# Kernel optimization log

Measured on AMD Instinct MI355X. Metric: run time of the kernel, lower is better.

Reference implementation:

```python
import jax, jax.numpy as jnp
import numpy as np

N_CLUSTERS = 64
N_GHOST = 2
EPS = 1e-12  # F.normalize eps


def setup_inputs() -> dict:
    key = jax.random.key(0)
    k1, k2, k3, k4 = jax.random.split(key, 4)
    n_utts, feat_dim, duration = 16, 256, 1500
    x = jax.random.normal(k1, (n_utts, feat_dim, duration), dtype=jnp.float32)
    centroids = jax.random.uniform(k2, (N_CLUSTERS, feat_dim), dtype=jnp.float32)
    # NetVLAD init ties linear.weight = 2*alpha*centroids(+ghosts); here independent params suffice for a math baseline
    lin_w = jax.random.normal(k3, (N_CLUSTERS + N_GHOST, feat_dim), dtype=jnp.float32)
    lin_b = jax.random.normal(k4, (N_CLUSTERS + N_GHOST,), dtype=jnp.float32)
    return {"x": x, "centroids": centroids, "lin_w": lin_w, "lin_b": lin_b}


def reference(x, centroids, lin_w, lin_b):
    # x: [u, f, t] -> [u, t, f]
    n_utts = x.shape[0]
    xt = jnp.transpose(x, (0, 2, 1))
    # soft assignments over clusters+ghosts, then drop ghost columns
    logits = jnp.einsum('utf,cf->utc', xt, lin_w) + lin_b  # [u,t,C+G]
    a = jax.nn.softmax(logits, axis=2)[..., :N_CLUSTERS]   # [u,t,C]
    # Fused NetVLAD aggregation (algebraically identical to
    # sum_t a[u,t,c] * (x[u,t,:] - centroids[c,:]) without materializing
    # the [u,t,C,f] residual tensor):
    comp = jnp.einsum('utc,utf->ucf', a, xt) - a.sum(axis=1)[..., None] * centroids  # [u,C,f]
    # intra-normalization (F.normalize p=2 over feat dim)
    comp = comp / jnp.maximum(jnp.linalg.norm(comp, axis=2, keepdims=True), EPS)
    sv = comp.reshape(n_utts, -1)  # [u, C*f]
    sv = sv / jnp.maximum(jnp.linalg.norm(sv, axis=1, keepdims=True), EPS)
    return sv
```

## Files before the change

### kernel.cpp

```cpp
#include <hip/hip_runtime.h>
#include <math.h>


#define NU 16
#define NF 256
#define NT 1500
#define NC 64
#define NCG 66
#define EPSN 1e-12f
#define TCH 96
#define NCHUNK 16

typedef float v2f __attribute__((ext_vector_type(2)));

#define S_WSM 24576
#define S_BUF 33288
#define S_TOT 39624

__device__ __forceinline__ int XS(int f, int k) {
    return f * 96 + (k ^ ((f & 15) << 1));
}

__global__ __launch_bounds__(512, 2) void ka_fused(
        const float* __restrict__ x, const float* __restrict__ lin_w,
        const float* __restrict__ lin_b, float* __restrict__ partial,
        float* __restrict__ asum_part) {
    __shared__ float S[S_TOT];
    float* Wsm = S + S_WSM;
    float* Buf = S + S_BUF;

    const int chunk = blockIdx.x, u = blockIdx.y;
    const int tid = threadIdx.x, lane = tid & 63, wave = tid >> 6;
    const int t0 = chunk * TCH;

    {
        const int fr = tid >> 3;
        const int ks = (tid & 7) * 4;
        #pragma unroll
        for (int r = 0; r < 4; ++r) {
            const int f = fr + 64 * r;
            const float* rp = x + (size_t)(u * NF + f) * NT + t0;
            #pragma unroll
            for (int q = 0; q < 3; ++q) {
                const int kk = ks + 32 * q;
                const int tg = t0 + kk;
                float4 v;
                if (tg + 3 < NT) v = *(const float4*)(rp + kk);
                else {
                    v.x = (tg + 0 < NT) ? rp[kk + 0] : 0.0f;
                    v.y = (tg + 1 < NT) ? rp[kk + 1] : 0.0f;
                    v.z = (tg + 2 < NT) ? rp[kk + 2] : 0.0f;
                    v.w = (tg + 3 < NT) ? rp[kk + 3] : 0.0f;
                }
                *(v2f*)&S[XS(f, kk)]     = (v2f){v.x, v.y};
                *(v2f*)&S[XS(f, kk + 2)] = (v2f){v.z, v.w};
            }
        }
        for (int i = tid; i < NCG * 128; i += 512) {
            const int c = i >> 7, k = i & 127;
            Wsm[c * 132 + k] = lin_w[c * NF + k];
        }
    }
    __syncthreads();

    const int nmy = (wave < 2) ? 9 : 8;
    const int c0  = (wave < 2) ? wave * 9 : 18 + (wave - 2) * 8;
    const int lp  = (lane < 48) ? lane : 47;

    v2f acc[9];
    #pragma unroll
    for (int i = 0; i < 9; ++i) acc[i] = (v2f){0.0f, 0.0f};

    #pragma unroll
    for (int kh = 0; kh < 2; ++kh) {
        #pragma unroll
        for (int fc = 0; fc < 8; ++fc) {
            const int fb = fc * 16;
            v2f xv[16];
            #pragma unroll
            for (int k2 = 0; k2 < 16; ++k2)
                xv[k2] = *(const v2f*)&S[XS(kh * 128 + fb + k2, 2 * lp)];
            #pragma unroll
            for (int i = 0; i < 9; ++i) {
                if (i < nmy) {
                    const float4* wp = (const float4*)&Wsm[(c0 + i) * 132 + fb];
                    const float4 w0 = wp[0], w1 = wp[1], w2 = wp[2], w3 = wp[3];
                    v2f a = acc[i];
                    a += xv[0]  * w0.x; a += xv[1]  * w0.y; a += xv[2]  * w0.z; a += xv[3]  * w0.w;
                    a += xv[4]  * w1.x; a += xv[5]  * w1.y; a += xv[6]  * w1.z; a += xv[7]  * w1.w;
                    a += xv[8]  * w2.x; a += xv[9]  * w2.y; a += xv[10] * w2.z; a += xv[11] * w2.w;
                    a += xv[12] * w3.x; a += xv[13] * w3.y; a += xv[14] * w3.z; a += xv[15] * w3.w;
                    acc[i] = a;
                }
            }
        }
        __syncthreads();
        if (kh == 0) {
            for (int i = tid; i < NCG * 128; i += 512) {
                const int c = i >> 7, k = i & 127;
                Wsm[c * 132 + k] = lin_w[c * NF + 128 + k];
            }
            __syncthreads();
        }
    }

    if (lane < 48) {
        #pragma unroll
        for (int i = 0; i < 9; ++i)
            if (i < nmy)
                *(v2f*)&Buf[(c0 + i) * 96 + 2 * lp] = acc[i];
    }
    __syncthreads();

    v2f mx = (v2f){-INFINITY, -INFINITY};
    #pragma unroll
    for (int c = 0; c < NCG; ++c) {
        const v2f l = *(const v2f*)&Buf[c * 96 + 2 * lp];
        const float b = lin_b[c];
        mx.x = fmaxf(mx.x, l.x + b); mx.y = fmaxf(mx.y, l.y + b);
    }
    v2f sm = (v2f){0.0f, 0.0f};
    #pragma unroll
    for (int c = 0; c < NCG; ++c) {
        const v2f l = *(const v2f*)&Buf[c * 96 + 2 * lp];
        const float b = lin_b[c];
        sm.x += __expf(l.x + b - mx.x);
        sm.y += __expf(l.y + b - mx.y);
    }
    const int tA = t0 + 2 * lp;
    const float sA = (tA     < NT) ? (1.0f / sm.x) : 0.0f;
    const float sB = (tA + 1 < NT) ? (1.0f / sm.y) : 0.0f;
    v2f aout[9];
    #pragma unroll
    for (int i = 0; i < 9; ++i) {
        const float b = lin_b[c0 + ((i < nmy) ? i : 0)];
        aout[i] = (v2f){__expf(acc[i].x + b - mx.x) * sA,
                        __expf(acc[i].y + b - mx.y) * sB};
    }
    __syncthreads();
    if (lane < 48) {
        #pragma unroll
        for (int i = 0; i < 9; ++i)
            if (i < nmy)
                *(v2f*)&Buf[(c0 + i) * 96 + 2 * lp] = aout[i];
    }
    __syncthreads();

    {
        const int cb = wave * 8;
        v2f ag[8][4], as[8];
        #pragma unroll
        for (int i = 0; i < 8; ++i) {
            as[i] = (v2f){0.0f, 0.0f};
            #pragma unroll
            for (int j = 0; j < 4; ++j) ag[i][j] = (v2f){0.0f, 0.0f};
        }
        for (int kp = 0; kp < TCH / 2; ++kp) {
            v2f av[8], xv2[4];
            #pragma unroll
            for (int i = 0; i < 8; ++i)
                av[i] = *(const v2f*)&Buf[(cb + i) * 96 + 2 * kp];
            #pragma unroll
            for (int j = 0; j < 4; ++j)
                xv2[j] = *(const v2f*)&S[XS(lane + 64 * j, 2 * kp)];
            #pragma unroll
            for (int i = 0; i < 8; ++i) {
                as[i] += av[i];
                #pragma unroll
                for (int j = 0; j < 4; ++j) ag[i][j] += av[i] * xv2[j];
            }
        }
        #pragma unroll
        for (int i = 0; i < 8; ++i) {
            float* op = partial + ((size_t)((chunk * NU + u) * NC + cb + i)) * NF;
            #pragma unroll
            for (int j = 0; j < 4; ++j) op[lane + 64 * j] = ag[i][j].x + ag[i][j].y;
        }
        if (lane == 0) {
            #pragma unroll
            for (int i = 0; i < 8; ++i)
                asum_part[(chunk * NU + u) * NC + cb + i] = as[i].x + as[i].y;
        }
    }
}

__global__ __launch_bounds__(1024) void kbc(
        const float* __restrict__ asum_part, const float* __restrict__ partial,
        const float* __restrict__ centroids, float* __restrict__ out) {
    const int u = blockIdx.x;
    const int tid = threadIdx.x, lane = tid & 63, wave = tid >> 6;
    __shared__ float rq[NC];

    float4 keep[4];
    float dinv[4];
    #pragma unroll
    for (int i = 0; i < 4; ++i) {
        const int c = wave + 16 * i;
        float asum = 0.0f;
        #pragma unroll
        for (int ch = 0; ch < NCHUNK; ++ch)
            asum += asum_part[(ch * NU + u) * NC + c];

        float4 val = make_float4(0.f, 0.f, 0.f, 0.f);
        #pragma unroll
        for (int ch = 0; ch < NCHUNK; ++ch) {
            const float4 p = *(const float4*)(
                partial + ((size_t)((ch * NU + u) * NC + c)) * NF + lane * 4);
            val.x += p.x; val.y += p.y; val.z += p.z; val.w += p.w;
        }
        const float4 ce = *(const float4*)(centroids + c * NF + lane * 4);
        val.x -= asum * ce.x; val.y -= asum * ce.y;
        val.z -= asum * ce.z; val.w -= asum * ce.w;

        float ss = val.x * val.x + val.y * val.y + val.z * val.z + val.w * val.w;
        #pragma unroll
        for (int off = 32; off > 0; off >>= 1) ss += __shfl_down(ss, off, 64);
        ss = __shfl(ss, 0, 64);

        const float d = fmaxf(sqrtf(ss), EPSN);
        keep[i] = val;
        dinv[i] = 1.0f / d;
        if (lane == 0) rq[c] = ss / (d * d);
    }
    __syncthreads();
    float g = 0.0f;
    #pragma unroll
    for (int c = 0; c < NC; ++c) g += rq[c];
    const float ginv = 1.0f / fmaxf(sqrtf(g), EPSN);
    #pragma unroll
    for (int i = 0; i < 4; ++i) {
        const int c = wave + 16 * i;
        const float sc = dinv[i] * ginv;
        float4 o = keep[i];
        o.x *= sc; o.y *= sc; o.z *= sc; o.w *= sc;
        *(float4*)(out + (size_t)u * (NC * NF) + c * NF + lane * 4) = o;
    }
}

extern "C" void kernel_launch(void* const* d_in, const int* in_sizes, int n_in,
                              void* d_out, int out_size, void* d_ws, size_t ws_size,
                              hipStream_t stream) {
    (void)in_sizes; (void)n_in; (void)out_size; (void)ws_size;
    const float* x         = (const float*)d_in[0];
    const float* centroids = (const float*)d_in[1];
    const float* lin_w     = (const float*)d_in[2];
    const float* lin_b     = (const float*)d_in[3];
    float* out = (float*)d_out;

    float* ws        = (float*)d_ws;
    float* partial   = ws;
    float* asum_part = partial + (size_t)NCHUNK * NU * NC * NF;

    hipLaunchKernelGGL(ka_fused, dim3(NCHUNK, NU), dim3(512), 0, stream,
                       x, lin_w, lin_b, partial, asum_part);
    hipLaunchKernelGGL(kbc, dim3(NU), dim3(1024), 0, stream,
                       asum_part, partial, centroids, out);
}
```

Baseline: 124.4 us.

## Split normalization kernel across clusters using constant global norm

Replaces the per-utterance 1024-thread normalization kernel with a 256-block grid where each wave handles one cluster row. Because every intra-normalized row has unit norm, the global L2 norm is fixed at sqrt(64), so the cross-cluster reduction and block sync are replaced by a constant 0.125 scale. This spreads the bandwidth-bound reduction of partial sums over many more CUs. It gives a different result only when a cluster residual is exactly zero, a degenerate case.

New measurement: 113.7 us. 8.6% less time.

```diff
diff --git a/kernel.cpp b/kernel.cpp
--- a/kernel.cpp
+++ b/kernel.cpp
@@ -10,6 +10,7 @@
 #define EPSN 1e-12f
 #define TCH 96
 #define NCHUNK 16
+#define GINV 0.125f
 
 typedef float v2f __attribute__((ext_vector_type(2)));
 
@@ -184,57 +185,38 @@
     }
 }
 
-__global__ __launch_bounds__(1024) void kbc(
+__global__ __launch_bounds__(256) void kb2(
         const float* __restrict__ asum_part, const float* __restrict__ partial,
         const float* __restrict__ centroids, float* __restrict__ out) {
-    const int u = blockIdx.x;
-    const int tid = threadIdx.x, lane = tid & 63, wave = tid >> 6;
-    __shared__ float rq[NC];
-
-    float4 keep[4];
-    float dinv[4];
-    #pragma unroll
-    for (int i = 0; i < 4; ++i) {
-        const int c = wave + 16 * i;
-        float asum = 0.0f;
-        #pragma unroll
-        for (int ch = 0; ch < NCHUNK; ++ch)
-            asum += asum_part[(ch * NU + u) * NC + c];
-
-        float4 val = make_float4(0.f, 0.f, 0.f, 0.f);
-        #pragma unroll
-        for (int ch = 0; ch < NCHUNK; ++ch) {
-            const float4 p = *(const float4*)(
-                partial + ((size_t)((ch * NU + u) * NC + c)) * NF + lane * 4);
-            val.x += p.x; val.y += p.y; val.z += p.z; val.w += p.w;
-        }
-        const float4 ce = *(const float4*)(centroids + c * NF + lane * 4);
-        val.x -= asum * ce.x; val.y -= asum * ce.y;
-        val.z -= asum * ce.z; val.w -= asum * ce.w;
-
-        float ss = val.x * val.x + val.y * val.y + val.z * val.z + val.w * val.w;
-        #pragma unroll
-        for (int off = 32; off > 0; off >>= 1) ss += __shfl_down(ss, off, 64);
-        ss = __shfl(ss, 0, 64);
-
-        const float d = fmaxf(sqrtf(ss), EPSN);
-        keep[i] = val;
-        dinv[i] = 1.0f / d;
-        if (lane == 0) rq[c] = ss / (d * d);
-    }
-    __syncthreads();
-    float g = 0.0f;
-    #pragma unroll
-    for (int c = 0; c < NC; ++c) g += rq[c];
-    const float ginv = 1.0f / fmaxf(sqrtf(g), EPSN);
-    #pragma unroll
-    for (int i = 0; i < 4; ++i) {
-        const int c = wave + 16 * i;
-        const float sc = dinv[i] * ginv;
-        float4 o = keep[i];
-        o.x *= sc; o.y *= sc; o.z *= sc; o.w *= sc;
-        *(float4*)(out + (size_t)u * (NC * NF) + c * NF + lane * 4) = o;
-    }
+    const int u = blockIdx.y;
+    const int wave = threadIdx.x >> 6, lane = threadIdx.x & 63;
+    const int c = blockIdx.x * 4 + wave;
+
+    float asum = 0.0f;
+    #pragma unroll
+    for (int ch = 0; ch < NCHUNK; ++ch)
+        asum += asum_part[(ch * NU + u) * NC + c];
+
+    float4 val = make_float4(0.f, 0.f, 0.f, 0.f);
+    #pragma unroll
+    for (int ch = 0; ch < NCHUNK; ++ch) {
+        const float4 p = *(const float4*)(
+            partial + ((size_t)((ch * NU + u) * NC + c)) * NF + lane * 4);
+        val.x += p.x; val.y += p.y; val.z += p.z; val.w += p.w;
+    }
+    const float4 ce = *(const float4*)(centroids + c * NF + lane * 4);
+    val.x -= asum * ce.x; val.y -= asum * ce.y;
+    val.z -= asum * ce.z; val.w -= asum * ce.w;
+
+    float ss = val.x * val.x + val.y * val.y + val.z * val.z + val.w * val.w;
+    #pragma unroll
+    for (int off = 32; off > 0; off >>= 1) ss += __shfl_down(ss, off, 64);
+    ss = __shfl(ss, 0, 64);
+
+    const float sc = GINV / fmaxf(sqrtf(ss), EPSN);
+    float4 o;
+    o.x = val.x * sc; o.y = val.y * sc; o.z = val.z * sc; o.w = val.w * sc;
+    *(float4*)(out + (size_t)u * (NC * NF) + c * NF + lane * 4) = o;
 }
 
 extern "C" void kernel_launch(void* const* d_in, const int* in_sizes, int n_in,
@@ -253,6 +235,6 @@
 
     hipLaunchKernelGGL(ka_fused, dim3(NCHUNK, NU), dim3(512), 0, stream,
                        x, lin_w, lin_b, partial, asum_part);
-    hipLaunchKernelGGL(kbc, dim3(NU), dim3(1024), 0, stream,
+    hipLaunchKernelGGL(kb2, dim3(16, NU), dim3(256), 0, stream,
                        asum_part, partial, centroids, out);
 }
```
